# Kernel optimization log

Hardware: AMD Instinct MI355X
Metric: run time of the kernel (lower is better)

The kernel has to match this reference:

```python
import jax, jax.numpy as jnp
import numpy as np

N = 192      # num_tracklets
D = 4096     # feature dim (hardcoded in original forward via expand(..., 4096))


def setup_inputs() -> dict:
    key = jax.random.key(0)
    ks = jax.random.split(key, 8)
    s = 0.02
    f   = jax.random.normal(ks[0], (N, D), jnp.float32)
    # learned parameters (torch Linear convention: W [out, in], y = x @ W.T + b)
    Wc1 = jax.random.normal(ks[1], (D, D),    jnp.float32) * s
    bc1 = jnp.zeros((D,), jnp.float32)
    W1  = jax.random.normal(ks[2], (2048, D), jnp.float32) * s
    b1  = jnp.zeros((2048,), jnp.float32)
    W2  = jax.random.normal(ks[3], (1024, 2048), jnp.float32) * s
    b2  = jnp.zeros((1024,), jnp.float32)
    W3  = jax.random.normal(ks[4], (512, 1024), jnp.float32) * s
    b3  = jnp.zeros((512,), jnp.float32)
    Ws  = jax.random.normal(ks[5], (1, 512), jnp.float32) * s
    bs  = jnp.zeros((1,), jnp.float32)
    return {"f": f, "Wc1": Wc1, "bc1": bc1, "W1": W1, "b1": b1,
            "W2": W2, "b2": b2, "W3": W3, "b3": b3, "Ws": Ws, "bs": bs}


def reference(f, Wc1, bc1, W1, b1, W2, b2, W3, b3, Ws, bs):
    # camera-feature removal: f <- f - relu(cam_fc1(f))
    cam = jax.nn.relu(f @ Wc1.T + bc1)            # [N, D]
    g = f - cam                                   # [N, D]
    # pairwise broadcast abs-diff: [N, N, D]
    dist = jnp.abs(g[:, None, :] - g[None, :, :])
    # 3-layer MLP affinity head + sigmoid
    h = jax.nn.relu(jnp.einsum('ijd,kd->ijk', dist, W1) + b1)   # [N, N, 2048]
    h = jax.nn.relu(h @ W2.T + b2)                              # [N, N, 1024]
    h = jax.nn.relu(h @ W3.T + b3)                              # [N, N, 512]
    A = jax.nn.sigmoid(h @ Ws.T + bs)[..., 0]                   # [N, N]
    return A
```

## Files before the change

### kernel.cpp

```cpp
#include <hip/hip_runtime.h>
#include <hip/hip_bf16.h>


typedef unsigned short u16;
typedef __attribute__((ext_vector_type(8))) short    bf16x8;
typedef __attribute__((ext_vector_type(8))) unsigned short u16x8;
typedef __attribute__((ext_vector_type(4))) float    f32x4;

#define MFMA16(a, b, c) __builtin_amdgcn_mfma_f32_16x16x32_bf16((a), (b), (c), 0, 0, 0)

#define NTRK 192
#define TRI  18528
#define TRIP 18688

__device__ __forceinline__ unsigned int pkbf(float lo, float hi) {
    __hip_bfloat162 h2 = __float22bfloat162_rn(make_float2(lo, hi));
    return *reinterpret_cast<unsigned int*>(&h2);
}
__device__ __forceinline__ void gll16(void* lds_uniform, const void* gsrc) {
    __builtin_amdgcn_global_load_lds(
        (__attribute__((address_space(1))) void*)(gsrc),
        (__attribute__((address_space(3))) void*)(lds_uniform),
        16, 0, 0);
}
__device__ __forceinline__ void tri_decode(int r, int& oi, int& oj) {
    double a = 192.5;
    int i = (int)(a - sqrt(a * a - 2.0 * (double)r));
    i = i < 0 ? 0 : (i > 191 ? 191 : i);
    while (i < 191 && (i + 1) * (385 - (i + 1)) / 2 <= r) ++i;
    while (i > 0 && i * (385 - i) / 2 > r) --i;
    int j = i + (r - i * (385 - i) / 2);
    oi = i; oj = j > 191 ? 191 : j;
}

__global__ __launch_bounds__(256)
void k_cvt(const float* __restrict__ src, u16* __restrict__ dst, int n4)
{
    int i = blockIdx.x * blockDim.x + threadIdx.x;
    const int stride = gridDim.x * blockDim.x;
    for (; i < n4; i += stride) {
        f32x4 v = ((const f32x4*)src)[i];
        ((uint2*)dst)[i] = make_uint2(pkbf(v.x, v.y), pkbf(v.z, v.w));
    }
}

__global__ __launch_bounds__(256, 2)
void k_cam(const u16* __restrict__ fb, const u16* __restrict__ Wc1b,
           const float* __restrict__ bc1, const float* __restrict__ f,
           float* __restrict__ gout)
{
    __shared__ __align__(16) u16 As[64 * 64];
    __shared__ __align__(16) u16 Bs[128 * 64];
    const int t = threadIdx.x, l = t & 63, w = t >> 6;
    const int m0 = blockIdx.x * 64, n0 = blockIdx.y * 128;
    const int lr8 = l >> 3;
    const int lc8 = (l & 7) ^ lr8;
    const u16* Ab = fb   + (size_t)(m0 + w * 16 + lr8) * 4096 + lc8 * 8;
    const u16* Bb = Wc1b + (size_t)(n0 + w * 32 + lr8) * 4096 + lc8 * 8;
    f32x4 acc[2][4] = {};
    const int wr = (w >> 1) * 32, wc = (w & 1) * 64;
    const int lrow = l & 15, lq = l >> 4, s = lrow & 7;

    for (int k0 = 0; k0 < 4096; k0 += 64) {
        __syncthreads();
#pragma unroll
        for (int q = 0; q < 2; ++q)
            gll16(&As[(w * 16 + q * 8) * 64], Ab + (size_t)q * 8 * 4096 + k0);
#pragma unroll
        for (int q = 0; q < 4; ++q)
            gll16(&Bs[(w * 32 + q * 8) * 64], Bb + (size_t)q * 8 * 4096 + k0);
        __syncthreads();
#pragma unroll
        for (int kk8 = 0; kk8 < 8; kk8 += 4) {
            const int co = ((kk8 + lq) ^ s) * 8;
            bf16x8 af[2], bfr[4];
#pragma unroll
            for (int mi = 0; mi < 2; ++mi)
                af[mi] = *(const bf16x8*)&As[(wr + mi * 16 + lrow) * 64 + co];
#pragma unroll
            for (int ni = 0; ni < 4; ++ni)
                bfr[ni] = *(const bf16x8*)&Bs[(wc + ni * 16 + lrow) * 64 + co];
#pragma unroll
            for (int mi = 0; mi < 2; ++mi)
#pragma unroll
                for (int ni = 0; ni < 4; ++ni)
                    acc[mi][ni] = MFMA16(af[mi], bfr[ni], acc[mi][ni]);
        }
    }
    const int rq = (l >> 4) * 4;
#pragma unroll
    for (int ni = 0; ni < 4; ++ni) {
        const int col = n0 + wc + ni * 16 + lrow;
        const float bias = bc1[col];
#pragma unroll
        for (int mi = 0; mi < 2; ++mi) {
            const int rbase = m0 + wr + mi * 16 + rq;
#pragma unroll
            for (int v = 0; v < 4; ++v) {
                const int row = rbase + v;
                float cam = fmaxf(acc[mi][ni][v] + bias, 0.0f);
                gout[(size_t)row * 4096 + col] = f[(size_t)row * 4096 + col] - cam;
            }
        }
    }
}

__global__ __launch_bounds__(256)
void k_distgen(const float* __restrict__ g, u16* __restrict__ dist, int row0)
{
    const int r = blockIdx.y;
    const int c = blockIdx.x * 256 + threadIdx.x;
    int pi, pj; tri_decode(row0 + r, pi, pj);
    const float* gi = g + (size_t)pi * 4096 + c * 8;
    const float* gj = g + (size_t)pj * 4096 + c * 8;
    f32x4 a0 = ((const f32x4*)gi)[0], a1 = ((const f32x4*)gi)[1];
    f32x4 b0 = ((const f32x4*)gj)[0], b1 = ((const f32x4*)gj)[1];
    uint4 o;
    o.x = pkbf(fabsf(b0.x - a0.x), fabsf(b0.y - a0.y));
    o.y = pkbf(fabsf(b0.z - a0.z), fabsf(b0.w - a0.w));
    o.z = pkbf(fabsf(b1.x - a1.x), fabsf(b1.y - a1.y));
    o.w = pkbf(fabsf(b1.z - a1.z), fabsf(b1.w - a1.w));
    *reinterpret_cast<uint4*>(dist + (size_t)r * 4096 + c * 8) = o;
}

__global__ __launch_bounds__(256, 2)
void k_gemm_relu(const u16* __restrict__ A, const u16* __restrict__ B,
                 const float* __restrict__ bias, u16* __restrict__ C,
                 int N, int K)
{
    __shared__ __align__(16) u16 As[128 * 64];
    __shared__ __align__(16) u16 Bs[128 * 64];
    const int t = threadIdx.x, l = t & 63, w = t >> 6;
    const int m0 = blockIdx.y * 128, n0 = blockIdx.x * 128;
    const int lr8 = l >> 3;
    const int lc8 = (l & 7) ^ lr8;
    const u16* Ab = A + (size_t)(m0 + w * 32 + lr8) * K + lc8 * 8;
    const u16* Bb = B + (size_t)(n0 + w * 32 + lr8) * K + lc8 * 8;
    f32x4 acc[4][4] = {};
    const int wr = (w >> 1) * 64, wc = (w & 1) * 64;
    const int lrow = l & 15, lq = l >> 4, s = lrow & 7;

    for (int k0 = 0; k0 < K; k0 += 64) {
        __syncthreads();
#pragma unroll
        for (int q = 0; q < 4; ++q) {
            gll16(&As[(w * 32 + q * 8) * 64], Ab + (size_t)q * 8 * K + k0);
            gll16(&Bs[(w * 32 + q * 8) * 64], Bb + (size_t)q * 8 * K + k0);
        }
        __syncthreads();
#pragma unroll
        for (int kk8 = 0; kk8 < 8; kk8 += 4) {
            const int co = ((kk8 + lq) ^ s) * 8;
            bf16x8 af[4], bfr[4];
#pragma unroll
            for (int mi = 0; mi < 4; ++mi)
                af[mi] = *(const bf16x8*)&As[(wr + mi * 16 + lrow) * 64 + co];
#pragma unroll
            for (int ni = 0; ni < 4; ++ni)
                bfr[ni] = *(const bf16x8*)&Bs[(wc + ni * 16 + lrow) * 64 + co];
#pragma unroll
            for (int mi = 0; mi < 4; ++mi)
#pragma unroll
                for (int ni = 0; ni < 4; ++ni)
                    acc[mi][ni] = MFMA16(af[mi], bfr[ni], acc[mi][ni]);
        }
    }
    const int rq = (l >> 4) * 4;
#pragma unroll
    for (int ni = 0; ni < 4; ++ni) {
        const int col = n0 + wc + ni * 16 + lrow;
        const float bv = bias[col];
#pragma unroll
        for (int mi = 0; mi < 4; ++mi) {
            const int rbase = m0 + wr + mi * 16 + rq;
#pragma unroll
            for (int v = 0; v < 4; ++v) {
                float x = fmaxf(acc[mi][ni][v] + bv, 0.0f);
                C[(size_t)(rbase + v) * N + col] = (u16)(pkbf(x, 0.0f) & 0xFFFF);
            }
        }
    }
}

__global__ __launch_bounds__(256)
void k_head(const u16* __restrict__ h3, const float* __restrict__ Wsv,
            const float* __restrict__ bsv, float* __restrict__ out, int row0)
{
    const int t = threadIdx.x, l = t & 63, wv = t >> 6;
    const int rl = blockIdx.x * 4 + wv;
    if (row0 + rl >= TRI) return;
    const u16x8 hv = *(const u16x8*)(h3 + (size_t)rl * 512 + l * 8);
    const f32x4 w0 = ((const f32x4*)Wsv)[l * 2];
    const f32x4 w1 = ((const f32x4*)Wsv)[l * 2 + 1];
    float hs[8];
#pragma unroll
    for (int e = 0; e < 8; ++e) {
        union { unsigned int i; float f; } v;
        v.i = ((unsigned int)hv[e]) << 16;
        hs[e] = v.f;
    }
    float s = hs[0] * w0.x + hs[1] * w0.y + hs[2] * w0.z + hs[3] * w0.w
            + hs[4] * w1.x + hs[5] * w1.y + hs[6] * w1.z + hs[7] * w1.w;
#pragma unroll
    for (int off = 32; off >= 1; off >>= 1) s += __shfl_down(s, off, 64);
    if (l == 0) {
        float v = 1.0f / (1.0f + __expf(-(s + bsv[0])));
        int pi, pj; tri_decode(row0 + rl, pi, pj);
        out[pi * NTRK + pj] = v;
        out[pj * NTRK + pi] = v;
    }
}

extern "C" void kernel_launch(void* const* d_in, const int* in_sizes, int n_in,
                              void* d_out, int out_size, void* d_ws, size_t ws_size,
                              hipStream_t stream)
{
    const float* f   = (const float*)d_in[0];
    const float* Wc1 = (const float*)d_in[1];
    const float* bc1 = (const float*)d_in[2];
    const float* W1  = (const float*)d_in[3];
    const float* b1  = (const float*)d_in[4];
    const float* W2  = (const float*)d_in[5];
    const float* b2  = (const float*)d_in[6];
    const float* W3  = (const float*)d_in[7];
    const float* b3  = (const float*)d_in[8];
    const float* Wsv = (const float*)d_in[9];
    const float* bsv = (const float*)d_in[10];
    float* out = (float*)d_out;

    char* wsb = (char*)d_ws;
    size_t off = 0;
    u16* Wc1b = (u16*)(wsb + off); off += (size_t)4096 * 4096 * 2;
    u16* W1b  = (u16*)(wsb + off); off += (size_t)2048 * 4096 * 2;
    u16* W2b  = (u16*)(wsb + off); off += (size_t)1024 * 2048 * 2;
    u16* W3b  = (u16*)(wsb + off); off += (size_t)512  * 1024 * 2;
    u16* fb   = (u16*)(wsb + off); off += (size_t)192  * 4096 * 2;
    float* g  = (float*)(wsb + off); off += (size_t)192 * 4096 * 4;
    const size_t fixed = off;

    const int Rcand[6] = {18688, 9344, 4736, 2432, 1280, 384};
    int R = 128;
    for (int c = 0; c < 6; ++c) {
        size_t need = fixed + (size_t)Rcand[c] * 15360;
        if (need <= ws_size) { R = Rcand[c]; break; }
    }
    u16* dist = (u16*)(wsb + fixed);
    u16* h1 = dist + (size_t)R * 4096;
    u16* h2 = h1 + (size_t)R * 2048;
    u16* h3 = h2 + (size_t)R * 1024;

    k_cvt<<<512, 256, 0, stream>>>(Wc1, Wc1b, 4096 * 4096 / 4);
    k_cvt<<<512, 256, 0, stream>>>(W1,  W1b,  2048 * 4096 / 4);
    k_cvt<<<256, 256, 0, stream>>>(W2,  W2b,  1024 * 2048 / 4);
    k_cvt<<<128, 256, 0, stream>>>(W3,  W3b,  512  * 1024 / 4);
    k_cvt<<<128, 256, 0, stream>>>(f,   fb,   192  * 4096 / 4);

    k_cam<<<dim3(3, 32), 256, 0, stream>>>(fb, Wc1b, bc1, f, g);

    for (int r0 = 0; r0 < TRI; r0 += R) {
        int rows = TRIP - r0; if (rows > R) rows = R;
        k_distgen<<<dim3(2, rows), 256, 0, stream>>>(g, dist, r0);
        k_gemm_relu<<<dim3(16, rows / 128), 256, 0, stream>>>(dist, W1b, b1, h1, 2048, 4096);
        k_gemm_relu<<<dim3(8,  rows / 128), 256, 0, stream>>>(h1, W2b, b2, h2, 1024, 2048);
        k_gemm_relu<<<dim3(4,  rows / 128), 256, 0, stream>>>(h2, W3b, b3, h3, 512, 1024);
        k_head<<<dim3(rows / 4), 256, 0, stream>>>(h3, Wsv, bsv, out, r0);
    }
}
```

Baseline: 748.6 us.

## Split-K the camera GEMM, fuse weight conversions, and alias workspace buffers

Merges the five fp32-to-bf16 conversion launches into one kernel with a flat grid. The camera GEMM now splits K four ways (384 blocks instead of 96) to fill more CUs, writes fp32 partials, and a new k_gfin kernel sums them with bias, ReLU and subtraction. Workspace is reorganised: Wc1b overlaps the dist/h chunk region and h2 aliases dist, so larger R chunks fit. This adds partial-sum traffic and an extra launch.

```diff
diff --git a/kernel.cpp b/kernel.cpp
--- a/kernel.cpp
+++ b/kernel.cpp
@@ -33,26 +33,35 @@
     oi = i; oj = j > 191 ? 191 : j;
 }
 
-__global__ __launch_bounds__(256)
-void k_cvt(const float* __restrict__ src, u16* __restrict__ dst, int n4)
-{
-    int i = blockIdx.x * blockDim.x + threadIdx.x;
-    const int stride = gridDim.x * blockDim.x;
-    for (; i < n4; i += stride) {
-        f32x4 v = ((const f32x4*)src)[i];
-        ((uint2*)dst)[i] = make_uint2(pkbf(v.x, v.y), pkbf(v.z, v.w));
-    }
+#define CVT_N 7143424
+__global__ __launch_bounds__(256)
+void k_cvt_all(const float* __restrict__ s0, u16* __restrict__ d0,
+               const float* __restrict__ s1, u16* __restrict__ d1,
+               const float* __restrict__ s2, u16* __restrict__ d2,
+               const float* __restrict__ s3, u16* __restrict__ d3,
+               const float* __restrict__ s4, u16* __restrict__ d4)
+{
+    int i = blockIdx.x * 256 + threadIdx.x;
+    if (i >= CVT_N) return;
+    const float* s; u16* d; int j;
+    if      (i < 4194304) { s = s0; d = d0; j = i; }
+    else if (i < 6291456) { s = s1; d = d1; j = i - 4194304; }
+    else if (i < 6815744) { s = s2; d = d2; j = i - 6291456; }
+    else if (i < 6946816) { s = s3; d = d3; j = i - 6815744; }
+    else                  { s = s4; d = d4; j = i - 6946816; }
+    f32x4 v = ((const f32x4*)s)[j];
+    ((uint2*)d)[j] = make_uint2(pkbf(v.x, v.y), pkbf(v.z, v.w));
 }
 
 __global__ __launch_bounds__(256, 2)
 void k_cam(const u16* __restrict__ fb, const u16* __restrict__ Wc1b,
-           const float* __restrict__ bc1, const float* __restrict__ f,
-           float* __restrict__ gout)
+           float* __restrict__ camp)
 {
     __shared__ __align__(16) u16 As[64 * 64];
     __shared__ __align__(16) u16 Bs[128 * 64];
     const int t = threadIdx.x, l = t & 63, w = t >> 6;
     const int m0 = blockIdx.x * 64, n0 = blockIdx.y * 128;
+    const int kbeg = blockIdx.z * 1024, kend = kbeg + 1024;
     const int lr8 = l >> 3;
     const int lc8 = (l & 7) ^ lr8;
     const u16* Ab = fb   + (size_t)(m0 + w * 16 + lr8) * 4096 + lc8 * 8;
@@ -61,7 +70,7 @@
     const int wr = (w >> 1) * 32, wc = (w & 1) * 64;
     const int lrow = l & 15, lq = l >> 4, s = lrow & 7;
 
-    for (int k0 = 0; k0 < 4096; k0 += 64) {
+    for (int k0 = kbeg; k0 < kend; k0 += 64) {
         __syncthreads();
 #pragma unroll
         for (int q = 0; q < 2; ++q)
@@ -87,22 +96,39 @@
                     acc[mi][ni] = MFMA16(af[mi], bfr[ni], acc[mi][ni]);
         }
     }
+    float* cz = camp + (size_t)blockIdx.z * 192 * 4096;
     const int rq = (l >> 4) * 4;
 #pragma unroll
     for (int ni = 0; ni < 4; ++ni) {
         const int col = n0 + wc + ni * 16 + lrow;
-        const float bias = bc1[col];
 #pragma unroll
         for (int mi = 0; mi < 2; ++mi) {
             const int rbase = m0 + wr + mi * 16 + rq;
 #pragma unroll
-            for (int v = 0; v < 4; ++v) {
-                const int row = rbase + v;
-                float cam = fmaxf(acc[mi][ni][v] + bias, 0.0f);
-                gout[(size_t)row * 4096 + col] = f[(size_t)row * 4096 + col] - cam;
-            }
-        }
-    }
+            for (int v = 0; v < 4; ++v)
+                cz[(size_t)(rbase + v) * 4096 + col] = acc[mi][ni][v];
+        }
+    }
+}
+
+__global__ __launch_bounds__(256)
+void k_gfin(const float* __restrict__ camp, const float* __restrict__ bc1,
+            const float* __restrict__ f, float* __restrict__ g)
+{
+    const int i = blockIdx.x * 256 + threadIdx.x;
+    const int col4 = (i * 4) & 4095;
+    f32x4 p0 = ((const f32x4*)camp)[i];
+    f32x4 p1 = ((const f32x4*)(camp + 786432))[i];
+    f32x4 p2 = ((const f32x4*)(camp + 1572864))[i];
+    f32x4 p3 = ((const f32x4*)(camp + 2359296))[i];
+    f32x4 b = *(const f32x4*)(bc1 + col4);
+    f32x4 fv = ((const f32x4*)f)[i];
+    f32x4 r;
+    r.x = fv.x - fmaxf(p0.x + p1.x + p2.x + p3.x + b.x, 0.0f);
+    r.y = fv.y - fmaxf(p0.y + p1.y + p2.y + p3.y + b.y, 0.0f);
+    r.z = fv.z - fmaxf(p0.z + p1.z + p2.z + p3.z + b.z, 0.0f);
+    r.w = fv.w - fmaxf(p0.w + p1.w + p2.w + p3.w + b.w, 0.0f);
+    ((f32x4*)g)[i] = r;
 }
 
 __global__ __launch_bounds__(256)
@@ -230,32 +256,32 @@
 
     char* wsb = (char*)d_ws;
     size_t off = 0;
-    u16* Wc1b = (u16*)(wsb + off); off += (size_t)4096 * 4096 * 2;
-    u16* W1b  = (u16*)(wsb + off); off += (size_t)2048 * 4096 * 2;
-    u16* W2b  = (u16*)(wsb + off); off += (size_t)1024 * 2048 * 2;
-    u16* W3b  = (u16*)(wsb + off); off += (size_t)512  * 1024 * 2;
-    u16* fb   = (u16*)(wsb + off); off += (size_t)192  * 4096 * 2;
-    float* g  = (float*)(wsb + off); off += (size_t)192 * 4096 * 4;
-    const size_t fixed = off;
-
-    const int Rcand[6] = {18688, 9344, 4736, 2432, 1280, 384};
+    u16*   W1b  = (u16*)(wsb + off);  off += (size_t)2048 * 4096 * 2;
+    u16*   W2b  = (u16*)(wsb + off);  off += (size_t)1024 * 2048 * 2;
+    u16*   W3b  = (u16*)(wsb + off);  off += (size_t)512  * 1024 * 2;
+    u16*   fb   = (u16*)(wsb + off);  off += (size_t)192  * 4096 * 2;
+    float* g    = (float*)(wsb + off); off += (size_t)192 * 4096 * 4;
+    float* camp = (float*)(wsb + off); off += (size_t)4 * 192 * 4096 * 4;
+    const size_t chunkbase = off;
+    u16* Wc1b = (u16*)(wsb + chunkbase);
+    const size_t wc1b_bytes = (size_t)4096 * 4096 * 2;
+
+    const int Rcand[6] = {18688, 9344, 4736, 2432, 1280, 640};
     int R = 128;
     for (int c = 0; c < 6; ++c) {
-        size_t need = fixed + (size_t)Rcand[c] * 15360;
-        if (need <= ws_size) { R = Rcand[c]; break; }
-    }
-    u16* dist = (u16*)(wsb + fixed);
+        size_t chunk = (size_t)Rcand[c] * 12288;
+        if (chunk < wc1b_bytes) chunk = wc1b_bytes;
+        if (chunkbase + chunk <= ws_size) { R = Rcand[c]; break; }
+    }
+    u16* dist = (u16*)(wsb + chunkbase);
     u16* h1 = dist + (size_t)R * 4096;
-    u16* h2 = h1 + (size_t)R * 2048;
+    u16* h2 = dist;
     u16* h3 = h2 + (size_t)R * 1024;
 
-    k_cvt<<<512, 256, 0, stream>>>(Wc1, Wc1b, 4096 * 4096 / 4);
-    k_cvt<<<512, 256, 0, stream>>>(W1,  W1b,  2048 * 4096 / 4);
-    k_cvt<<<256, 256, 0, stream>>>(W2,  W2b,  1024 * 2048 / 4);
-    k_cvt<<<128, 256, 0, stream>>>(W3,  W3b,  512  * 1024 / 4);
-    k_cvt<<<128, 256, 0, stream>>>(f,   fb,   192  * 4096 / 4);
-
-    k_cam<<<dim3(3, 32), 256, 0, stream>>>(fb, Wc1b, bc1, f, g);
+    k_cvt_all<<<(CVT_N + 255) / 256, 256, 0, stream>>>(
+        Wc1, Wc1b, W1, W1b, W2, W2b, W3, W3b, f, fb);
+    k_cam<<<dim3(3, 32, 4), 256, 0, stream>>>(fb, Wc1b, camp);
+    k_gfin<<<768, 256, 0, stream>>>(camp, bc1, f, g);
 
     for (int r0 = 0; r0 < TRI; r0 += R) {
         int rows = TRIP - r0; if (rows > R) rows = R;
```

Result: faster. 732.5 us (-2.2%).
